# Kernel optimization log

Hardware: AMD Instinct MI355X
Metric: run time of the kernel (lower is better)

## Reference

```python
import jax, jax.numpy as jnp
import numpy as np

N_NODES = 200000
N_EDGES = 800000
N_GRAPHS = 8192
NFEAT = 74
FP = 1024
H = 4   # num heads
F = 50  # feats per head
BN_EPS = 1e-5
ATTN_SLOPE = 0.2     # GATConv leaky-relu alpha
ACT_SLOPE = 0.01     # nn.LeakyReLU() default after layer 1
CAPS_COEF = 1.0 / np.sqrt(128.0)  # 1/sqrt(D), D=128


def squash2(x, axis=-1):
    sq = (x ** 2).sum(axis=axis, keepdims=True)
    return (1.0 - 1.0 / jnp.exp(jnp.sqrt(sq))) * x / jnp.sqrt(sq + 1e-8)


def gat_layer(x, src, dst, W, attn_l, attn_r, bias, res_W):
    # x: [N, in] -> feat: [N, H, F]
    feat = (x @ W).reshape(N_NODES, H, F)
    el = (feat * attn_l).sum(-1)            # [N, H]
    er = (feat * attn_r).sum(-1)            # [N, H]
    e = jax.nn.leaky_relu(el[src] + er[dst], ATTN_SLOPE)  # [E, H]
    # edge softmax over incoming edges of each dst node
    m = jax.ops.segment_max(e, dst, num_segments=N_NODES)
    a = jnp.exp(e - m[dst])
    denom = jax.ops.segment_sum(a, dst, num_segments=N_NODES)
    alpha = a / denom[dst]                  # [E, H]
    out = jax.ops.segment_sum(alpha[:, :, None] * feat[src], dst,
                              num_segments=N_NODES)  # [N, H, F]
    if res_W is None:
        res = x.reshape(N_NODES, H, F)      # identity residual (in == H*F)
    else:
        res = (x @ res_W).reshape(N_NODES, H, F)
    return out + res + bias.reshape(1, H, F)


def setup_inputs():
    key = jax.random.key(0)
    ks = jax.random.split(key, 24)
    h = jax.random.normal(ks[0], (N_NODES, NFEAT), jnp.float32)
    fps = (jax.random.uniform(ks[1], (N_GRAPHS, FP)) < 0.1).astype(jnp.float32)
    src = jax.random.randint(ks[2], (N_EDGES,), 0, N_NODES)
    dst = jax.random.randint(ks[3], (N_EDGES,), 0, N_NODES)
    # sorted graph assignment, every graph non-empty
    graph_id = (jnp.arange(N_NODES) * N_GRAPHS) // N_NODES
    s = 0.05
    p = lambda i, shp: s * jax.random.normal(ks[i], shp, jnp.float32)
    return dict(
        h=h, fps=fps, src=src, dst=dst, graph_id=graph_id,
        W1=p(4, (NFEAT, H * F)), al1=p(5, (H, F)), ar1=p(6, (H, F)),
        b1=p(7, (H * F,)), resW1=p(8, (NFEAT, H * F)),
        W2=p(9, (H * F, H * F)), al2=p(10, (H, F)), ar2=p(11, (H, F)),
        b2=p(12, (H * F,)),
        lw1=p(13, (F + FP, 128)), lb1=p(14, (128,)),
        bn_g=jnp.ones((128,), jnp.float32), bn_b=jnp.zeros((128,), jnp.float32),
        bn_rm=jnp.zeros((128,), jnp.float32), bn_rv=jnp.ones((128,), jnp.float32),
        lw2=p(15, (128, 128)), lb2=p(16, (128,)),
        capsW=0.01 * jax.random.normal(ks[17], (2, 16, 2, 8), jnp.float32),
        capsB=0.01 * jax.random.normal(ks[18], (2, 1, 16), jnp.float32),
    )


def reference(h, fps, src, dst, graph_id, W1, al1, ar1, b1, resW1,
              W2, al2, ar2, b2, lw1, lb1, bn_g, bn_b, bn_rm, bn_rv,
              lw2, lb2, capsW, capsB):
    # ---- GAT layer 1: flatten heads + LeakyReLU ----
    x = gat_layer(h, src, dst, W1, al1, ar1, b1, resW1).reshape(N_NODES, H * F)
    x = jax.nn.leaky_relu(x, ACT_SLOPE)
    # ---- GAT layer 2: mean over heads, no activation ----
    x = gat_layer(x, src, dst, W2, al2, ar2, b2, None).mean(axis=1)  # [N, F]
    # ---- MaxPooling per graph ----
    g = jax.ops.segment_max(x, graph_id, num_segments=N_GRAPHS)  # [G, F]
    # ---- MLP head (eval mode: dropout off, BN uses running stats) ----
    z = jnp.concatenate([g, fps], axis=-1)
    z = jax.nn.relu(z @ lw1 + lb1)
    z = (z - bn_rm) / jnp.sqrt(bn_rv + BN_EPS) * bn_g + bn_b
    z = jax.nn.relu(z @ lw2 + lb2)                                # [G, 128]
    # ---- PrimaryCaps2: view (G, 16, 8), squash ----
    u = squash2(z.reshape(N_GRAPHS, 16, 8))
    # ---- DigitCaps2 ----
    # u_hat[b,n,c,d] = sum_e W[n,c,d,e] * u[b,c,e]
    u_hat = jnp.einsum('ncde,bce->bncd', capsW, u)                # [G,2,16,2]
    a = CAPS_COEF * jnp.einsum('bncd,bnkd->bnck', u_hat, u_hat)   # [G,2,16,16]
    c = jax.nn.softmax(a.sum(axis=-2, keepdims=True), axis=1)     # [G,2,1,16]
    s = jnp.matmul(c + capsB, u_hat).squeeze(-2)                  # [G,2,2]
    v = squash2(s)
    return jnp.sqrt((v ** 2).sum(-1) + 1e-8)                      # [G,2]
```

## Files before the change

### kernel.cpp

```cpp
#include <hip/hip_runtime.h>
#include <hip/hip_bf16.h>

#define NN 200000
#define NE 800000
#define NG 8192
#define KIN 74
#define FPD 1024
#define HF 200
#define FF 50

typedef float f4 __attribute__((ext_vector_type(4)));
typedef __hip_bfloat16 bf16;
typedef __attribute__((ext_vector_type(8))) short sh8;
typedef __attribute__((ext_vector_type(4))) float f32x4;

__device__ __forceinline__ unsigned short f2bf(float f) {
    unsigned u = __float_as_uint(f);
    u += 0x7fffu + ((u >> 16) & 1u);
    return (unsigned short)(u >> 16);
}
__device__ __forceinline__ float bflo(unsigned u) { return __uint_as_float(u << 16); }
__device__ __forceinline__ float bfhi(unsigned u) { return __uint_as_float(u & 0xffff0000u); }
__device__ __forceinline__ unsigned pack2(float a, float b) {
    return (unsigned)f2bf(a) | ((unsigned)f2bf(b) << 16);
}

__global__ __launch_bounds__(256)
void k_prep_a(const float* __restrict__ h, unsigned* __restrict__ hp)
{
    int idx = blockIdx.x * 256 + threadIdx.x;
    if (idx >= NN * 48) return;
    int row = idx / 48, c2 = idx - row * 48;
    int k = 2 * c2;
    float v0 = (k     < KIN) ? h[(size_t)row * KIN + k]     : 0.f;
    float v1 = (k + 1 < KIN) ? h[(size_t)row * KIN + k + 1] : 0.f;
    hp[idx] = pack2(v0, v1);
}

__global__ __launch_bounds__(256)
void k_prep_bt(const float* __restrict__ W, unsigned short* __restrict__ Bt,
               int K, int N, int kPad, int colOff)
{
    int idx = blockIdx.x * 256 + threadIdx.x;
    if (idx >= 208 * kPad) return;
    int col = idx / kPad, k = idx - col * kPad;
    float v = (col < N && k < K) ? W[(size_t)k * N + col] : 0.f;
    Bt[(size_t)(colOff + col) * kPad + k] = f2bf(v);
}

template<int KCH>
__global__ __launch_bounds__(256)
void gemm_mfma(const unsigned short* __restrict__ A, int lda,
               const unsigned short* __restrict__ Bt,
               const float* __restrict__ bias2,
               bf16* __restrict__ C1, bf16* __restrict__ C2)
{
    const int t = threadIdx.x;
    const int lane = t & 63, w = t >> 6;
    const int l15 = lane & 15, l4 = lane >> 4;
    const int kPad = KCH * 32;
    const int mat = blockIdx.y;
    const int row0 = blockIdx.x * 64 + w * 16;
    const unsigned short* ap = A + (size_t)(row0 + l15) * lda + l4 * 8;
    const unsigned short* bp = Bt + (size_t)mat * 208 * kPad
                                  + (size_t)l15 * kPad + l4 * 8;
    f32x4 acc[13] = {};

    #pragma unroll 2
    for (int kc = 0; kc < KCH; ++kc) {
        sh8 a = *(const sh8*)(ap + kc * 32);
        #pragma unroll
        for (int ct = 0; ct < 13; ++ct) {
            sh8 b = *(const sh8*)(bp + (size_t)ct * 16 * kPad + kc * 32);
            acc[ct] = __builtin_amdgcn_mfma_f32_16x16x32_bf16(a, b, acc[ct], 0, 0, 0);
        }
    }

    bf16* C = mat ? C2 : C1;
    const bool hasb = (mat == 1) && (bias2 != nullptr);
    #pragma unroll
    for (int ct = 0; ct < 13; ++ct) {
        int col = ct * 16 + l15;
        if (col < 200) {
            float bv = hasb ? bias2[col] : 0.f;
            #pragma unroll
            for (int j = 0; j < 4; ++j) {
                int row = row0 + l4 * 4 + j;
                C[(size_t)row * 200 + col] = __float2bfloat16(acc[ct][j] + bv);
            }
        }
    }
}

template<int MODE>
__global__ __launch_bounds__(256)
void gemm_tile(const float* __restrict__ A, const float* __restrict__ A2,
               const float* __restrict__ B1,
               const float* __restrict__ bias,
               const float* __restrict__ bng, const float* __restrict__ bnb,
               const float* __restrict__ bnrm, const float* __restrict__ bnrv,
               float* __restrict__ C1f, int M, int K)
{
    __shared__ float As[16][68];
    __shared__ float Bs[16][64];
    const int t = threadIdx.x;
    const int tx = t & 15, ty = t >> 4;
    const int r0 = blockIdx.y * 64, c0 = blockIdx.x * 64;
    float acc[4][4] = {};
    const int arow = t >> 2;
    const int akl  = (t & 3) * 4;
    const int bkl  = t >> 4;
    const int bcl  = (t & 15) * 4;

    for (int kk = 0; kk < K; kk += 16) {
        const int r = r0 + arow;
        #pragma unroll
        for (int i = 0; i < 4; ++i) {
            int k = kk + akl + i;
            float v = 0.f;
            if (k < K && r < M) {
                if (MODE == 2) v = (k < 50) ? A[(size_t)r*50 + k] : A2[(size_t)r*1024 + (k - 50)];
                else           v = A[(size_t)r*K + k];
            }
            As[akl + i][arow] = v;
        }
        const int kb = kk + bkl;
        #pragma unroll
        for (int i = 0; i < 4; ++i) {
            int c = c0 + bcl + i;
            float v = 0.f;
            if (kb < K && c < 128) v = B1[(size_t)kb*128 + c];
            Bs[bkl][bcl + i] = v;
        }
        __syncthreads();
        #pragma unroll
        for (int k = 0; k < 16; ++k) {
            f4 av = *(const f4*)&As[k][ty*4];
            f4 bv = *(const f4*)&Bs[k][tx*4];
            #pragma unroll
            for (int i = 0; i < 4; ++i)
                #pragma unroll
                for (int j = 0; j < 4; ++j)
                    acc[i][j] += av[i] * bv[j];
        }
        __syncthreads();
    }

    #pragma unroll
    for (int i = 0; i < 4; ++i) {
        int r = r0 + ty*4 + i;
        if (r >= M) continue;
        #pragma unroll
        for (int j = 0; j < 4; ++j) {
            int c = c0 + tx*4 + j;
            if (c >= 128) continue;
            float v = acc[i][j] + bias[c];
            if (MODE == 2) {
                v = fmaxf(v, 0.f);
                v = (v - bnrm[c]) * rsqrtf(bnrv[c] + 1e-5f) * bng[c] + bnb[c];
            } else {
                v = fmaxf(v, 0.f);
            }
            C1f[(size_t)r*128 + c] = v;
        }
    }
}

__global__ __launch_bounds__(256)
void k_el_er(const bf16* __restrict__ feat,
             const float* __restrict__ al, const float* __restrict__ ar,
             float* __restrict__ el, float* __restrict__ er)
{
    int t = blockIdx.x * 256 + threadIdx.x;
    if (t >= NN * 4) return;
    int n = t >> 2, h = t & 3;
    const unsigned* fr = (const unsigned*)(feat + (size_t)n*HF) + h*25;
    const float* alp = al + h*FF;
    const float* arp = ar + h*FF;
    float sl = 0.f, sr = 0.f;
    #pragma unroll
    for (int i = 0; i < 25; ++i) {
        unsigned u = fr[i];
        float v0 = bflo(u), v1 = bfhi(u);
        sl += v0*alp[2*i] + v1*alp[2*i+1];
        sr += v0*arp[2*i] + v1*arp[2*i+1];
    }
    el[t] = sl; er[t] = sr;
}

__global__ __launch_bounds__(256)
void k_count(const int* __restrict__ dst, int* __restrict__ cnt)
{
    int e = blockIdx.x * 256 + threadIdx.x;
    if (e < NE) atomicAdd(&cnt[dst[e]], 1);
}

__global__ __launch_bounds__(256)
void k_scan_a(const int* __restrict__ cnt, int* __restrict__ offs, int* __restrict__ bsum)
{
    __shared__ int tmp[256];
    int t = threadIdx.x, i = blockIdx.x * 256 + t;
    int v = (i < NN) ? cnt[i] : 0;
    tmp[t] = v; __syncthreads();
    #pragma unroll
    for (int d = 1; d < 256; d <<= 1) {
        int add = (t >= d) ? tmp[t - d] : 0; __syncthreads();
        tmp[t] += add; __syncthreads();
    }
    if (i < NN) offs[i + 1] = tmp[t];
    if (t == 255) bsum[blockIdx.x] = tmp[255];
}

__global__ __launch_bounds__(1024)
void k_scan_b(int* __restrict__ bsum, int nb)
{
    __shared__ int tmp[1024];
    int t = threadIdx.x;
    tmp[t] = (t < nb) ? bsum[t] : 0; __syncthreads();
    #pragma unroll
    for (int d = 1; d < 1024; d <<= 1) {
        int add = (t >= d) ? tmp[t - d] : 0; __syncthreads();
        tmp[t] += add; __syncthreads();
    }
    if (t < nb) bsum[t] = (t == 0) ? 0 : tmp[t - 1];
}

__global__ __launch_bounds__(256)
void k_scan_c(const int* __restrict__ bsum, int* __restrict__ offs)
{
    int i = blockIdx.x * 256 + threadIdx.x;
    if (i < NN) offs[i + 1] += bsum[blockIdx.x];
    if (i == 0) offs[0] = 0;
}

__global__ __launch_bounds__(256)
void k_fill(const int* __restrict__ src, const int* __restrict__ dst,
            const int* __restrict__ offs,
            int* __restrict__ cnt, int* __restrict__ csr_s)
{
    int e = blockIdx.x * 256 + threadIdx.x;
    if (e >= NE) return;
    int d = dst[e];
    int p = offs[d] + atomicAdd(&cnt[d], 1);
    csr_s[p] = src[e];
}

template<int LAYER>
__global__ __launch_bounds__(256)
void k_gather(const int* __restrict__ offs, const int* __restrict__ csr_s,
              const f4* __restrict__ el4, const f4* __restrict__ er4,
              const bf16* __restrict__ feat, const bf16* __restrict__ resx,
              const float* __restrict__ b2,
              bf16* __restrict__ x1out, bf16* __restrict__ x2out)
{
    __shared__ float sb[4][204];
    const int wv   = threadIdx.x >> 6;
    const int lane = threadIdx.x & 63;
    const int wid  = blockIdx.x * 4 + wv;
    const int beg = offs[wid], end = offs[wid + 1];
    const int hl  = (lane >= 25) ? 1 : 0;
    const bool act = lane < 50;

    const f4 erv = er4[wid];
    const float er_lo = hl ? erv.y : erv.x;
    const float er_hi = hl ? erv.w : erv.z;

    float s_lo = 0.f, s_hi = 0.f;
    float a0 = 0.f, a1 = 0.f, a2 = 0.f, a3 = 0.f;

#define EDGE(ev, lo, hi) {                                                  \
        float xl = (hl ? (ev).y : (ev).x) + er_lo;                          \
        xl = xl >= 0.f ? xl : 0.2f * xl;                                    \
        float xh = (hl ? (ev).w : (ev).z) + er_hi;                          \
        xh = xh >= 0.f ? xh : 0.2f * xh;                                    \
        float wl = __builtin_expf(xl), wh = __builtin_expf(xh);             \
        s_lo += wl; s_hi += wh;                                             \
        a0 += wl * bflo(lo); a1 += wl * bfhi(lo);                           \
        a2 += wh * bflo(hi); a3 += wh * bfhi(hi); }

    int i = beg;
    for (; i + 4 <= end; i += 4) {
        const int sn0 = csr_s[i], sn1 = csr_s[i+1], sn2 = csr_s[i+2], sn3 = csr_s[i+3];
        const f4 ev0 = el4[sn0], ev1 = el4[sn1], ev2 = el4[sn2], ev3 = el4[sn3];
        unsigned lo0=0, lo1=0, lo2=0, lo3=0, hi0=0, hi1=0, hi2=0, hi3=0;
        if (act) {
            const unsigned* f0 = (const unsigned*)(feat + (size_t)sn0 * HF);
            const unsigned* f1 = (const unsigned*)(feat + (size_t)sn1 * HF);
            const unsigned* f2 = (const unsigned*)(feat + (size_t)sn2 * HF);
            const unsigned* f3 = (const unsigned*)(feat + (size_t)sn3 * HF);
            lo0 = f0[lane]; hi0 = f0[lane + 50];
            lo1 = f1[lane]; hi1 = f1[lane + 50];
            lo2 = f2[lane]; hi2 = f2[lane + 50];
            lo3 = f3[lane]; hi3 = f3[lane + 50];
        }
        EDGE(ev0, lo0, hi0) EDGE(ev1, lo1, hi1) EDGE(ev2, lo2, hi2) EDGE(ev3, lo3, hi3)
    }
    for (; i < end; ++i) {
        const int sn = csr_s[i];
        const f4 ev = el4[sn];
        unsigned lo = 0, hi = 0;
        if (act) {
            const unsigned* fr = (const unsigned*)(feat + (size_t)sn * HF);
            lo = fr[lane]; hi = fr[lane + 50];
        }
        EDGE(ev, lo, hi)
    }
#undef EDGE

    const float inv_lo = s_lo > 0.f ? 1.f / s_lo : 0.f;
    const float inv_hi = s_hi > 0.f ? 1.f / s_hi : 0.f;
    a0 *= inv_lo; a1 *= inv_lo; a2 *= inv_hi; a3 *= inv_hi;

    if (LAYER == 1) {
        if (act) {
            const unsigned* rr = (const unsigned*)(resx + (size_t)wid * HF);
            unsigned rlo = rr[lane], rhi = rr[lane + 50];
            float t0 = a0 + bflo(rlo), t1 = a1 + bfhi(rlo);
            float t2 = a2 + bflo(rhi), t3 = a3 + bfhi(rhi);
            t0 = t0 >= 0.f ? t0 : 0.01f * t0;
            t1 = t1 >= 0.f ? t1 : 0.01f * t1;
            t2 = t2 >= 0.f ? t2 : 0.01f * t2;
            t3 = t3 >= 0.f ? t3 : 0.01f * t3;
            unsigned* xo = (unsigned*)(x1out + (size_t)wid * HF);
            xo[lane]      = pack2(t0, t1);
            xo[lane + 50] = pack2(t2, t3);
        }
    } else {
        if (act) {
            const unsigned* rr = (const unsigned*)(resx + (size_t)wid * HF);
            unsigned rlo = rr[lane], rhi = rr[lane + 50];
            int j = 2 * lane;
            sb[wv][j]       = a0 + bflo(rlo) + b2[j];
            sb[wv][j + 1]   = a1 + bfhi(rlo) + b2[j + 1];
            sb[wv][j + 100] = a2 + bflo(rhi) + b2[j + 100];
            sb[wv][j + 101] = a3 + bfhi(rhi) + b2[j + 101];
        }
        __syncthreads();
        if (lane < 25) {
            int j = 2 * lane;
            float v0 = 0.25f * (sb[wv][j]   + sb[wv][j + 50] + sb[wv][j + 100] + sb[wv][j + 150]);
            float v1 = 0.25f * (sb[wv][j+1] + sb[wv][j + 51] + sb[wv][j + 101] + sb[wv][j + 151]);
            unsigned* xo = (unsigned*)(x2out + (size_t)wid * FF);
            xo[lane] = pack2(v0, v1);
        }
    }
}

__global__ __launch_bounds__(64)
void k_graph_max(const bf16* __restrict__ x2, float* __restrict__ gp)
{
    int g = blockIdx.x;
    int f = threadIdx.x;
    if (f >= FF) return;
    long start = ((long)g     * NN + NG - 1) / NG;
    long end   = ((long)(g+1) * NN + NG - 1) / NG;
    float mv = -3.4e38f;
    for (long n = start; n < end; ++n) mv = fmaxf(mv, __bfloat162float(x2[n*FF + f]));
    gp[(size_t)g*FF + f] = mv;
}

__global__ __launch_bounds__(256)
void k_caps(const float* __restrict__ z2, const float* __restrict__ capsW,
            const float* __restrict__ capsB, float* __restrict__ out)
{
    int g = blockIdx.x * 256 + threadIdx.x;
    if (g >= NG) return;
    const float* z = z2 + (size_t)g*128;
    float uh[2][16][2];
    #pragma unroll
    for (int c = 0; c < 16; ++c) {
        float x[8]; float sq = 0.f;
        #pragma unroll
        for (int e = 0; e < 8; ++e) { x[e] = z[c*8 + e]; sq += x[e]*x[e]; }
        float sn  = sqrtf(sq);
        float fct = (1.f - __builtin_expf(-sn)) / sqrtf(sq + 1e-8f);
        #pragma unroll
        for (int e = 0; e < 8; ++e) x[e] *= fct;
        #pragma unroll
        for (int n = 0; n < 2; ++n)
            #pragma unroll
            for (int d = 0; d < 2; ++d) {
                float s2 = 0.f;
                #pragma unroll
                for (int e = 0; e < 8; ++e) s2 += capsW[((n*16 + c)*2 + d)*8 + e] * x[e];
                uh[n][c][d] = s2;
            }
    }
    float asum[2][16];
    #pragma unroll
    for (int n = 0; n < 2; ++n) {
        float t0 = 0.f, t1 = 0.f;
        #pragma unroll
        for (int c = 0; c < 16; ++c) { t0 += uh[n][c][0]; t1 += uh[n][c][1]; }
        #pragma unroll
        for (int k = 0; k < 16; ++k)
            asum[n][k] = 0.08838834764831845f * (t0*uh[n][k][0] + t1*uh[n][k][1]);
    }
    float s[2][2] = {};
    #pragma unroll
    for (int k = 0; k < 16; ++k) {
        float m  = fmaxf(asum[0][k], asum[1][k]);
        float e0 = __builtin_expf(asum[0][k] - m);
        float e1 = __builtin_expf(asum[1][k] - m);
        float inv = 1.f / (e0 + e1);
        float c0 = e0*inv + capsB[k];
        float c1 = e1*inv + capsB[16 + k];
        s[0][0] += c0*uh[0][k][0]; s[0][1] += c0*uh[0][k][1];
        s[1][0] += c1*uh[1][k][0]; s[1][1] += c1*uh[1][k][1];
    }
    #pragma unroll
    for (int n = 0; n < 2; ++n) {
        float sq  = s[n][0]*s[n][0] + s[n][1]*s[n][1];
        float sn  = sqrtf(sq);
        float fct = (1.f - __builtin_expf(-sn)) / sqrtf(sq + 1e-8f);
        float v0 = fct*s[n][0], v1 = fct*s[n][1];
        out[g*2 + n] = sqrtf(v0*v0 + v1*v1 + 1e-8f);
    }
}

extern "C" void kernel_launch(void* const* d_in, const int* in_sizes, int n_in,
                              void* d_out, int out_size, void* d_ws, size_t ws_size,
                              hipStream_t stream)
{
    const float* h     = (const float*)d_in[0];
    const float* fps   = (const float*)d_in[1];
    const int*   src   = (const int*)d_in[2];
    const int*   dst   = (const int*)d_in[3];
    const float* W1    = (const float*)d_in[5];
    const float* al1   = (const float*)d_in[6];
    const float* ar1   = (const float*)d_in[7];
    const float* b1    = (const float*)d_in[8];
    const float* resW1 = (const float*)d_in[9];
    const float* W2    = (const float*)d_in[10];
    const float* al2   = (const float*)d_in[11];
    const float* ar2   = (const float*)d_in[12];
    const float* b2    = (const float*)d_in[13];
    const float* lw1   = (const float*)d_in[14];
    const float* lb1   = (const float*)d_in[15];
    const float* bn_g  = (const float*)d_in[16];
    const float* bn_b  = (const float*)d_in[17];
    const float* bn_rm = (const float*)d_in[18];
    const float* bn_rv = (const float*)d_in[19];
    const float* lw2   = (const float*)d_in[20];
    const float* lb2   = (const float*)d_in[21];
    const float* capsW = (const float*)d_in[22];
    const float* capsB = (const float*)d_in[23];
    float* out = (float*)d_out;

    const int NB1 = (NN + 255) / 256;

    char* w = (char*)d_ws;
    auto alloc = [&](size_t nbytes) { char* p = w; w += (nbytes + 255) & ~(size_t)255; return p; };
    bf16* featb = (bf16*)alloc((size_t)NN*HF*2);
    bf16* x1b   = (bf16*)alloc((size_t)NN*HF*2);
    bf16* x2b   = (bf16*)alloc((size_t)NN*FF*2);
    unsigned* hpad = (unsigned*)alloc((size_t)NN*48*4);
    float* el   = (float*)alloc((size_t)NN*4*4);
    float* er   = (float*)alloc((size_t)NN*4*4);
    int*  offs  = (int*)alloc((size_t)(NN+1)*4);
    int*  cnt   = (int*)alloc((size_t)NN*4);
    int*  bsum  = (int*)alloc((size_t)NB1*4);
    int*  csr_s = (int*)alloc((size_t)NE*4);
    float* gp   = (float*)alloc((size_t)NG*FF*4);
    float* z1   = (float*)alloc((size_t)NG*128*4);
    float* z2   = (float*)alloc((size_t)NG*128*4);
    unsigned short* bt1 = (unsigned short*)alloc((size_t)416*96*2);
    unsigned short* bt2 = (unsigned short*)alloc((size_t)208*224*2);

    if ((size_t)(w - (char*)d_ws) > ws_size) return;

    const dim3 B256(256);

    hipLaunchKernelGGL(k_prep_a, dim3((NN*48+255)/256), B256, 0, stream, h, hpad);
    hipLaunchKernelGGL(k_prep_bt, dim3((208*96+255)/256),  B256, 0, stream, W1,    bt1, KIN, 200, 96, 0);
    hipLaunchKernelGGL(k_prep_bt, dim3((208*96+255)/256),  B256, 0, stream, resW1, bt1, KIN, 200, 96, 208);
    hipLaunchKernelGGL(k_prep_bt, dim3((208*224+255)/256), B256, 0, stream, W2,    bt2, HF, 200, 224, 0);

    hipMemsetAsync(cnt, 0, (size_t)NN*4, stream);
    hipLaunchKernelGGL(k_count,  dim3(3125), B256, 0, stream, dst, cnt);
    hipLaunchKernelGGL(k_scan_a, dim3(NB1),  B256, 0, stream, cnt, offs, bsum);
    hipLaunchKernelGGL(k_scan_b, dim3(1), dim3(1024), 0, stream, bsum, NB1);
    hipLaunchKernelGGL(k_scan_c, dim3(NB1),  B256, 0, stream, bsum, offs);
    hipMemsetAsync(cnt, 0, (size_t)NN*4, stream);
    hipLaunchKernelGGL(k_fill,   dim3(3125), B256, 0, stream, src, dst, offs, cnt, csr_s);

    hipLaunchKernelGGL((gemm_mfma<3>), dim3(3125, 2), B256, 0, stream,
        (const unsigned short*)hpad, 96, bt1, b1, featb, x1b);
    hipLaunchKernelGGL(k_el_er, dim3(3125), B256, 0, stream, featb, al1, ar1, el, er);
    hipLaunchKernelGGL((k_gather<1>), dim3(50000), B256, 0, stream,
        offs, csr_s, (const f4*)el, (const f4*)er, featb, x1b, nullptr, x1b, nullptr);

    hipLaunchKernelGGL((gemm_mfma<7>), dim3(3125, 1), B256, 0, stream,
        (const unsigned short*)x1b, 200, bt2, nullptr, featb, nullptr);
    hipLaunchKernelGGL(k_el_er, dim3(3125), B256, 0, stream, featb, al2, ar2, el, er);
    hipLaunchKernelGGL((k_gather<2>), dim3(50000), B256, 0, stream,
        offs, csr_s, (const f4*)el, (const f4*)er, featb, x1b, b2, nullptr, x2b);

    hipLaunchKernelGGL(k_graph_max, dim3(NG), dim3(64), 0, stream, x2b, gp);
    hipLaunchKernelGGL((gemm_tile<2>), dim3(2, 128), B256, 0, stream,
        gp, fps, lw1, lb1, bn_g, bn_b, bn_rm, bn_rv, z1, NG, 1074);
    hipLaunchKernelGGL((gemm_tile<3>), dim3(2, 128), B256, 0, stream,
        z1, nullptr, lw2, lb2, nullptr, nullptr, nullptr, nullptr, z2, NG, 128);
    hipLaunchKernelGGL(k_caps, dim3(32), B256, 0, stream, z2, capsW, capsB, out);
}
```

Before: 930.6 us.

## Move MLP head GEMMs to bf16 MFMA with split-K and fused epilogue

Replaces the fp32 LDS-tiled GEMMs of the MLP head with bf16 MFMA kernels. The concatenated [pooled, fps] input is packed into a padded bf16 buffer reusing workspace, and the first GEMM uses a 2-way split-K. A separate post kernel then sums the partials and applies bias, ReLU and batch norm. This aims to cut the scalar-FMA cost of the 8192x1074x128 GEMM, at the cost of bf16 rounding of the activations and extra packing and post kernels.

```diff
diff --git a/kernel.cpp b/kernel.cpp
--- a/kernel.cpp
+++ b/kernel.cpp
@@ -39,13 +39,25 @@
 
 __global__ __launch_bounds__(256)
 void k_prep_bt(const float* __restrict__ W, unsigned short* __restrict__ Bt,
-               int K, int N, int kPad, int colOff)
+               int K, int N, int kPad, int nColPad, int colOff)
 {
     int idx = blockIdx.x * 256 + threadIdx.x;
-    if (idx >= 208 * kPad) return;
+    if (idx >= nColPad * kPad) return;
     int col = idx / kPad, k = idx - col * kPad;
     float v = (col < N && k < K) ? W[(size_t)k * N + col] : 0.f;
     Bt[(size_t)(colOff + col) * kPad + k] = f2bf(v);
+}
+
+__global__ __launch_bounds__(256)
+void k_prep_fps(const float* __restrict__ fps, unsigned* __restrict__ zb)
+{
+    int idx = blockIdx.x * 256 + threadIdx.x;
+    if (idx >= NG * 519) return;
+    int g = idx / 519, dw = 25 + (idx - g * 519);
+    int c0 = 2 * dw - 50;
+    float v0 = (c0     < FPD) ? fps[(size_t)g * FPD + c0]     : 0.f;
+    float v1 = (c0 + 1 < FPD) ? fps[(size_t)g * FPD + c0 + 1] : 0.f;
+    zb[(size_t)g * 544 + dw] = pack2(v0, v1);
 }
 
 template<int KCH>
@@ -92,76 +104,91 @@
     }
 }
 
-template<int MODE>
-__global__ __launch_bounds__(256)
-void gemm_tile(const float* __restrict__ A, const float* __restrict__ A2,
-               const float* __restrict__ B1,
-               const float* __restrict__ bias,
-               const float* __restrict__ bng, const float* __restrict__ bnb,
-               const float* __restrict__ bnrm, const float* __restrict__ bnrv,
-               float* __restrict__ C1f, int M, int K)
-{
-    __shared__ float As[16][68];
-    __shared__ float Bs[16][64];
+__global__ __launch_bounds__(256)
+void gemm_mlp1(const unsigned short* __restrict__ A,
+               const unsigned short* __restrict__ Bt,
+               float* __restrict__ Cpart)
+{
     const int t = threadIdx.x;
-    const int tx = t & 15, ty = t >> 4;
-    const int r0 = blockIdx.y * 64, c0 = blockIdx.x * 64;
-    float acc[4][4] = {};
-    const int arow = t >> 2;
-    const int akl  = (t & 3) * 4;
-    const int bkl  = t >> 4;
-    const int bcl  = (t & 15) * 4;
-
-    for (int kk = 0; kk < K; kk += 16) {
-        const int r = r0 + arow;
-        #pragma unroll
-        for (int i = 0; i < 4; ++i) {
-            int k = kk + akl + i;
-            float v = 0.f;
-            if (k < K && r < M) {
-                if (MODE == 2) v = (k < 50) ? A[(size_t)r*50 + k] : A2[(size_t)r*1024 + (k - 50)];
-                else           v = A[(size_t)r*K + k];
-            }
-            As[akl + i][arow] = v;
-        }
-        const int kb = kk + bkl;
-        #pragma unroll
-        for (int i = 0; i < 4; ++i) {
-            int c = c0 + bcl + i;
-            float v = 0.f;
-            if (kb < K && c < 128) v = B1[(size_t)kb*128 + c];
-            Bs[bkl][bcl + i] = v;
-        }
-        __syncthreads();
-        #pragma unroll
-        for (int k = 0; k < 16; ++k) {
-            f4 av = *(const f4*)&As[k][ty*4];
-            f4 bv = *(const f4*)&Bs[k][tx*4];
-            #pragma unroll
-            for (int i = 0; i < 4; ++i)
-                #pragma unroll
-                for (int j = 0; j < 4; ++j)
-                    acc[i][j] += av[i] * bv[j];
-        }
-        __syncthreads();
-    }
-
-    #pragma unroll
-    for (int i = 0; i < 4; ++i) {
-        int r = r0 + ty*4 + i;
-        if (r >= M) continue;
+    const int lane = t & 63, w = t >> 6;
+    const int l15 = lane & 15, l4 = lane >> 4;
+    const int row0 = blockIdx.x * 64 + w * 16;
+    const int c0   = blockIdx.y * 64;
+    const int kz   = blockIdx.z;
+    const unsigned short* ap = A + (size_t)(row0 + l15) * 1088 + kz * 544 + l4 * 8;
+    const unsigned short* bp = Bt + (size_t)(c0 + l15) * 1088 + kz * 544 + l4 * 8;
+    f32x4 acc[4] = {};
+
+    #pragma unroll 2
+    for (int kc = 0; kc < 17; ++kc) {
+        sh8 a = *(const sh8*)(ap + kc * 32);
+        #pragma unroll
+        for (int ct = 0; ct < 4; ++ct) {
+            sh8 b = *(const sh8*)(bp + (size_t)ct * 16 * 1088 + kc * 32);
+            acc[ct] = __builtin_amdgcn_mfma_f32_16x16x32_bf16(a, b, acc[ct], 0, 0, 0);
+        }
+    }
+
+    float* Cp = Cpart + (size_t)kz * NG * 128;
+    #pragma unroll
+    for (int ct = 0; ct < 4; ++ct) {
+        int col = c0 + ct * 16 + l15;
         #pragma unroll
         for (int j = 0; j < 4; ++j) {
-            int c = c0 + tx*4 + j;
-            if (c >= 128) continue;
-            float v = acc[i][j] + bias[c];
-            if (MODE == 2) {
-                v = fmaxf(v, 0.f);
-                v = (v - bnrm[c]) * rsqrtf(bnrv[c] + 1e-5f) * bng[c] + bnb[c];
-            } else {
-                v = fmaxf(v, 0.f);
-            }
-            C1f[(size_t)r*128 + c] = v;
+            int row = row0 + l4 * 4 + j;
+            Cp[(size_t)row * 128 + col] = acc[ct][j];
+        }
+    }
+}
+
+__global__ __launch_bounds__(256)
+void k_mlp_post(const float* __restrict__ Cpart, const float* __restrict__ lb1,
+                const float* __restrict__ bng, const float* __restrict__ bnb,
+                const float* __restrict__ bnrm, const float* __restrict__ bnrv,
+                bf16* __restrict__ z1b)
+{
+    int i = blockIdx.x * 256 + threadIdx.x;
+    if (i >= NG * 128) return;
+    int c = i & 127;
+    float v = Cpart[i] + Cpart[(size_t)NG * 128 + i] + lb1[c];
+    v = fmaxf(v, 0.f);
+    v = (v - bnrm[c]) * rsqrtf(bnrv[c] + 1e-5f) * bng[c] + bnb[c];
+    z1b[i] = __float2bfloat16(v);
+}
+
+__global__ __launch_bounds__(256)
+void gemm_mlp2(const unsigned short* __restrict__ A,
+               const unsigned short* __restrict__ Bt,
+               const float* __restrict__ lb2,
+               float* __restrict__ z2)
+{
+    const int t = threadIdx.x;
+    const int lane = t & 63, w = t >> 6;
+    const int l15 = lane & 15, l4 = lane >> 4;
+    const int row0 = blockIdx.x * 64 + w * 16;
+    const int c0   = blockIdx.y * 64;
+    const unsigned short* ap = A + (size_t)(row0 + l15) * 128 + l4 * 8;
+    const unsigned short* bp = Bt + (size_t)(c0 + l15) * 128 + l4 * 8;
+    f32x4 acc[4] = {};
+
+    #pragma unroll
+    for (int kc = 0; kc < 4; ++kc) {
+        sh8 a = *(const sh8*)(ap + kc * 32);
+        #pragma unroll
+        for (int ct = 0; ct < 4; ++ct) {
+            sh8 b = *(const sh8*)(bp + (size_t)ct * 16 * 128 + kc * 32);
+            acc[ct] = __builtin_amdgcn_mfma_f32_16x16x32_bf16(a, b, acc[ct], 0, 0, 0);
+        }
+    }
+
+    #pragma unroll
+    for (int ct = 0; ct < 4; ++ct) {
+        int col = c0 + ct * 16 + l15;
+        float bv = lb2[col];
+        #pragma unroll
+        for (int j = 0; j < 4; ++j) {
+            int row = row0 + l4 * 4 + j;
+            z2[(size_t)row * 128 + col] = fmaxf(acc[ct][j] + bv, 0.f);
         }
     }
 }
@@ -347,7 +374,7 @@
 }
 
 __global__ __launch_bounds__(64)
-void k_graph_max(const bf16* __restrict__ x2, float* __restrict__ gp)
+void k_graph_max(const bf16* __restrict__ x2, bf16* __restrict__ zb)
 {
     int g = blockIdx.x;
     int f = threadIdx.x;
@@ -356,7 +383,7 @@
     long end   = ((long)(g+1) * NN + NG - 1) / NG;
     float mv = -3.4e38f;
     for (long n = start; n < end; ++n) mv = fmaxf(mv, __bfloat162float(x2[n*FF + f]));
-    gp[(size_t)g*FF + f] = mv;
+    zb[(size_t)g*1088 + f] = __float2bfloat16(mv);
 }
 
 __global__ __launch_bounds__(256)
@@ -461,20 +488,26 @@
     int*  cnt   = (int*)alloc((size_t)NN*4);
     int*  bsum  = (int*)alloc((size_t)NB1*4);
     int*  csr_s = (int*)alloc((size_t)NE*4);
-    float* gp   = (float*)alloc((size_t)NG*FF*4);
-    float* z1   = (float*)alloc((size_t)NG*128*4);
-    float* z2   = (float*)alloc((size_t)NG*128*4);
-    unsigned short* bt1 = (unsigned short*)alloc((size_t)416*96*2);
-    unsigned short* bt2 = (unsigned short*)alloc((size_t)208*224*2);
+    unsigned short* bt1  = (unsigned short*)alloc((size_t)416*96*2);
+    unsigned short* bt2  = (unsigned short*)alloc((size_t)208*224*2);
+    unsigned short* btm1 = (unsigned short*)alloc((size_t)128*1088*2);
+    unsigned short* btm2 = (unsigned short*)alloc((size_t)128*128*2);
+
+    unsigned* zb    = hpad;
+    float*    z1p   = (float*)(hpad + (size_t)NG*544);
+    bf16*     z1b   = (bf16*)((char*)z1p + (size_t)2*NG*128*4);
+    float*    z2    = (float*)((char*)z1b + (size_t)NG*128*2);
 
     if ((size_t)(w - (char*)d_ws) > ws_size) return;
 
     const dim3 B256(256);
 
     hipLaunchKernelGGL(k_prep_a, dim3((NN*48+255)/256), B256, 0, stream, h, hpad);
-    hipLaunchKernelGGL(k_prep_bt, dim3((208*96+255)/256),  B256, 0, stream, W1,    bt1, KIN, 200, 96, 0);
-    hipLaunchKernelGGL(k_prep_bt, dim3((208*96+255)/256),  B256, 0, stream, resW1, bt1, KIN, 200, 96, 208);
-    hipLaunchKernelGGL(k_prep_bt, dim3((208*224+255)/256), B256, 0, stream, W2,    bt2, HF, 200, 224, 0);
+    hipLaunchKernelGGL(k_prep_bt, dim3((208*96+255)/256),   B256, 0, stream, W1,    bt1,  KIN,  200,   96, 208, 0);
+    hipLaunchKernelGGL(k_prep_bt, dim3((208*96+255)/256),   B256, 0, stream, resW1, bt1,  KIN,  200,   96, 208, 208);
+    hipLaunchKernelGGL(k_prep_bt, dim3((208*224+255)/256),  B256, 0, stream, W2,    bt2,  HF,   200,  224, 208, 0);
+    hipLaunchKernelGGL(k_prep_bt, dim3((128*1088+255)/256), B256, 0, stream, lw1,   btm1, 1074, 128, 1088, 128, 0);
+    hipLaunchKernelGGL(k_prep_bt, dim3((128*128+255)/256),  B256, 0, stream, lw2,   btm2, 128,  128,  128, 128, 0);
 
     hipMemsetAsync(cnt, 0, (size_t)NN*4, stream);
     hipLaunchKernelGGL(k_count,  dim3(3125), B256, 0, stream, dst, cnt);
@@ -496,10 +529,13 @@
     hipLaunchKernelGGL((k_gather<2>), dim3(50000), B256, 0, stream,
         offs, csr_s, (const f4*)el, (const f4*)er, featb, x1b, b2, nullptr, x2b);
 
-    hipLaunchKernelGGL(k_graph_max, dim3(NG), dim3(64), 0, stream, x2b, gp);
-    hipLaunchKernelGGL((gemm_tile<2>), dim3(2, 128), B256, 0, stream,
-        gp, fps, lw1, lb1, bn_g, bn_b, bn_rm, bn_rv, z1, NG, 1074);
-    hipLaunchKernelGGL((gemm_tile<3>), dim3(2, 128), B256, 0, stream,
-        z1, nullptr, lw2, lb2, nullptr, nullptr, nullptr, nullptr, z2, NG, 128);
+    hipLaunchKernelGGL(k_graph_max, dim3(NG), dim3(64), 0, stream, x2b, (bf16*)zb);
+    hipLaunchKernelGGL(k_prep_fps, dim3((NG*519+255)/256), B256, 0, stream, fps, zb);
+    hipLaunchKernelGGL(gemm_mlp1, dim3(128, 2, 2), B256, 0, stream,
+        (const unsigned short*)zb, btm1, z1p);
+    hipLaunchKernelGGL(k_mlp_post, dim3((NG*128+255)/256), B256, 0, stream,
+        z1p, lb1, bn_g, bn_b, bn_rm, bn_rv, z1b);
+    hipLaunchKernelGGL(gemm_mlp2, dim3(128, 2), B256, 0, stream,
+        (const unsigned short*)z1b, btm2, lb2, z2);
     hipLaunchKernelGGL(k_caps, dim3(32), B256, 0, stream, z2, capsW, capsB, out);
 }
```

New measurement: 828.6 us. 11.0% less time.
